# Optimization experiments

Measured on AMD Instinct MI355X. Metric: run time of the kernel, lower is better.

The kernel has to match this reference:

```python
import jax, jax.numpy as jnp
import numpy as np

HIDDEN = 256
N_PROT = 12288
N_MOL = 6144
N_BATCH = 32


def setup_inputs() -> dict:
    key = jax.random.key(0)
    ks = jax.random.split(key, 10)
    s = 1.0 / np.sqrt(HIDDEN)  # torch Linear default init scale
    inp = {
        "prot_embed": jax.random.normal(ks[0], (N_PROT, HIDDEN), jnp.float32),
        "mol_embed": jax.random.normal(ks[1], (N_MOL, HIDDEN), jnp.float32),
        "prot_batch": jnp.sort(jax.random.randint(ks[2], (N_PROT,), 0, N_BATCH)),
        "mol_batch": jnp.sort(jax.random.randint(ks[3], (N_MOL,), 0, N_BATCH)),
        "Wq": jax.random.uniform(ks[4], (HIDDEN, HIDDEN), jnp.float32, -s, s),
        "bq": jax.random.uniform(ks[5], (HIDDEN,), jnp.float32, -s, s),
        "Wk": jax.random.uniform(ks[6], (HIDDEN, HIDDEN), jnp.float32, -s, s),
        "bk": jax.random.uniform(ks[7], (HIDDEN,), jnp.float32, -s, s),
        "Wv": jax.random.uniform(ks[8], (HIDDEN, HIDDEN), jnp.float32, -s, s),
        "bv": jax.random.uniform(ks[9], (HIDDEN,), jnp.float32, -s, s),
    }
    return inp


def reference(prot_embed, mol_embed, prot_batch, mol_batch, Wq, bq, Wk, bk, Wv, bv):
    # Linear projections (torch nn.Linear: x @ W.T + b)
    Q = prot_embed @ Wq.T + bq            # [N, H]
    K = mol_embed @ Wk.T + bk             # [M, H]
    V = mol_embed @ Wv.T + bv             # [M, H]

    scale = 1.0 / jnp.sqrt(jnp.asarray(Q.shape[-1], Q.dtype))
    scores = (Q @ K.T) * scale            # [N, M]

    # block mask: same-batch pairs only
    mask = prot_batch[:, None] == mol_batch[None, :]   # [N, M] bool
    neg_inf = jnp.asarray(-jnp.inf, scores.dtype)
    scores = jnp.where(mask, scores, neg_inf)

    # stable masked softmax; rows with no valid key -> all zeros
    # (matches torch softmax(-inf row) -> nan -> nan_to_num(0.0))
    row_any = mask.any(axis=-1, keepdims=True)
    mx = jnp.max(scores, axis=-1, keepdims=True)
    mx = jnp.where(row_any, mx, 0.0)
    e = jnp.exp(scores - mx)              # exp(-inf)=0 on masked entries
    denom = jnp.sum(e, axis=-1, keepdims=True)
    attn = e / jnp.where(row_any, denom, 1.0)  # [N, M]

    out = attn @ V                        # [N, H]
    return out, attn
```

## Files before the change

kernel.cpp:

```cpp
#include <hip/hip_runtime.h>

#define NPROT 12288
#define NMOL  6144
#define HID   256
#define NB    32

#define PROT_O 0
#define MOL_O  3145728
#define WQ_O   4718592
#define WK_O   4784128
#define WV_O   4849664
#define BQ_O   4915200
#define BK_O   4915456
#define BV_O   4915712
#define Q_O    4915968
#define K_O    8061696
#define VT_O   9634560
#define END_O  11207424

#define FILL_BLOCKS 512
#define FILL_CHUNK  73728
#define FILL_HALF   37748736

typedef __attribute__((ext_vector_type(4))) float f32x4;
typedef __attribute__((ext_vector_type(8))) short bf16x8;
typedef unsigned short u16;
typedef unsigned int   u32;

__device__ __forceinline__ float b2f(u16 u){
  union { u32 i; float f; } v; v.i = ((u32)u) << 16; return v.f;
}
__device__ __forceinline__ u16 f2b(float f){
  union { float fl; u32 i; } v; v.fl = f;
  u32 i = v.i;
  return (u16)((i + 0x7FFFu + ((i >> 16) & 1u)) >> 16);
}

__device__ __forceinline__ void fill_zero(float* attnf, int idx){
  float* dst = attnf + (size_t)idx * FILL_CHUNK + threadIdx.x * 4;
  f32x4 z = {0.f, 0.f, 0.f, 0.f};
  #pragma unroll 4
  for (int i = 0; i < 72; i++)
    __builtin_nontemporal_store(z, (f32x4*)(dst + i * 1024));
}

__global__ __launch_bounds__(256) void convert_kernel(
    const float* __restrict__ prot, const float* __restrict__ mol,
    const float* __restrict__ Wq, const float* __restrict__ Wk,
    const float* __restrict__ Wv, const float* __restrict__ bq,
    const float* __restrict__ bk, const float* __restrict__ bv,
    const int* __restrict__ pb, const int* __restrict__ mb,
    int* __restrict__ rg, u16* __restrict__ cvt, float* __restrict__ dout)
{
  if (blockIdx.x >= 4801){
    fill_zero(dout + (size_t)NPROT * HID, blockIdx.x - 4801);
    return;
  }
  int g = blockIdx.x * 256 + threadIdx.x;
  const float* src = nullptr; u16* dst = nullptr; int off = 0;
  if      (g < 786432)  { src = prot; dst = cvt + PROT_O; off = g; }
  else if (g < 1179648) { src = mol;  dst = cvt + MOL_O;  off = g - 786432; }
  else if (g < 1196032) { src = Wq;   dst = cvt + WQ_O;   off = g - 1179648; }
  else if (g < 1212416) { src = Wk;   dst = cvt + WK_O;   off = g - 1196032; }
  else if (g < 1228800) { src = Wv;   dst = cvt + WV_O;   off = g - 1212416; }
  else if (g < 1228864) { src = bq;   dst = cvt + BQ_O;   off = g - 1228800; }
  else if (g < 1228928) { src = bk;   dst = cvt + BK_O;   off = g - 1228864; }
  else if (g < 1228992) { src = bv;   dst = cvt + BV_O;   off = g - 1228928; }
  if (src){
    f32x4 v = *(const f32x4*)(src + (size_t)off * 4);
    ushort4 o;
    o.x = f2b(v[0]); o.y = f2b(v[1]); o.z = f2b(v[2]); o.w = f2b(v[3]);
    *(ushort4*)(dst + (size_t)off * 4) = o;
  }

  if (blockIdx.x == 0 && threadIdx.x < 64){
    int t = threadIdx.x;
    const int* arr = (t < 32) ? pb : mb;
    int n          = (t < 32) ? NPROT : NMOL;
    int target     = (t & 31) + 1;
    int lo = 0, hi = n;
    while (lo < hi){
      int mid = (lo + hi) >> 1;
      if (arr[mid] < target) lo = mid + 1; else hi = mid;
    }
    int end = lo;
    int prev = __shfl(end, t - 1);
    int start = ((t & 31) == 0) ? 0 : prev;
    int b = t & 31;
    if (t < 32){ rg[b] = start; rg[32 + b] = end; }
    else       { rg[64 + b] = start; rg[96 + b] = end; }
  }
}

__global__ __launch_bounds__(256) void proj_kernel(
    const u16* __restrict__ cvt,
    u16* __restrict__ Q, u16* __restrict__ K, u16* __restrict__ Vt,
    float* __restrict__ dout)
{
  __shared__ u16 tlds[4][64][18];
  if (blockIdx.x >= 1536){
    fill_zero(dout + (size_t)NPROT * HID + FILL_HALF, blockIdx.x - 1536);
    return;
  }
  int rowblk = blockIdx.x >> 2, colblk = blockIdx.x & 3;
  int proj;
  if      (rowblk < 192){ proj = 0; }
  else if (rowblk < 288){ proj = 1; rowblk -= 192; }
  else                  { proj = 2; rowblk -= 288; }
  const u16 *X, *W, *B;
  if (proj == 0){ X = cvt + PROT_O; W = cvt + WQ_O; B = cvt + BQ_O; }
  else if (proj == 1){ X = cvt + MOL_O; W = cvt + WK_O; B = cvt + BK_O; }
  else { X = cvt + MOL_O; W = cvt + WV_O; B = cvt + BV_O; }

  int wave = threadIdx.x >> 6, lane = threadIdx.x & 63;
  int m = lane & 15, q = lane >> 4;
  int rowbase = rowblk * 64 + wave * 16;
  int colbase = colblk * 64;

  const u16* arow = X + (size_t)(rowbase + m) * HID;
  f32x4 acc[4] = {};
  for (int k0 = 0; k0 < HID; k0 += 32){
    bf16x8 a = *(const bf16x8*)(arow + k0 + q*8);
    #pragma unroll
    for (int ct = 0; ct < 4; ct++){
      bf16x8 b = *(const bf16x8*)(W + (size_t)(colbase + ct*16 + m) * HID + k0 + q*8);
      acc[ct] = __builtin_amdgcn_mfma_f32_16x16x32_bf16(a, b, acc[ct], 0, 0, 0);
    }
  }

  if (proj < 2){
    u16* O = (proj == 0) ? Q : K;
    #pragma unroll
    for (int ct = 0; ct < 4; ct++){
      int col = colbase + ct*16 + m;
      float bb = b2f(B[col]);
      #pragma unroll
      for (int r = 0; r < 4; r++){
        int row = rowbase + q*4 + r;
        O[(size_t)row * HID + col] = f2b(acc[ct][r] + bb);
      }
    }
  } else {
    #pragma unroll
    for (int ct = 0; ct < 4; ct++){
      int lc = ct*16 + m;
      float bb = b2f(B[colbase + lc]);
      #pragma unroll
      for (int r = 0; r < 4; r++)
        tlds[wave][lc][q*4 + r] = f2b(acc[ct][r] + bb);
    }
    __syncthreads();
    int col = colbase + lane;
    u32 packed[8];
    #pragma unroll
    for (int i = 0; i < 8; i++){
      u16 lo = tlds[wave][lane][2*i];
      u16 hi = tlds[wave][lane][2*i+1];
      packed[i] = (u32)lo | ((u32)hi << 16);
    }
    u16* dst = Vt + (size_t)col * NMOL + rowbase;
    uint4 v0 = {packed[0], packed[1], packed[2], packed[3]};
    uint4 v1 = {packed[4], packed[5], packed[6], packed[7]};
    *(uint4*)dst = v0;
    *(uint4*)(dst + 8) = v1;
  }
}

__global__ __launch_bounds__(256) void attn_kernel(
    const int* __restrict__ rg, const u16* __restrict__ Q, const u16* __restrict__ K,
    const u16* __restrict__ Vt, float* __restrict__ dout)
{
  __shared__ u16 P[16][392];
  __shared__ float mxw[4][16];
  __shared__ float smw[4][16];
  const float scale = 0.0625f;
  int b = blockIdx.y;
  int ps = rg[b], pe = rg[32+b], ms = rg[64+b], me = rg[96+b];
  int Np = pe - ps, Nm = me - ms;
  if (Np <= 0) return;

  int wave = threadIdx.x >> 6, lane = threadIdx.x & 63;
  int m = lane & 15, q = lane >> 4;
  float* outf  = dout;
  float* attnf = dout + (size_t)NPROT * HID;
  int ntiles = (Np + 15) >> 4;

  int bs = 0, ce = 0;
  if (Nm > 0){ bs = ms & ~31; ce = bs + ((me - bs + 31) & ~31); }

  for (int tile = blockIdx.x; tile < ntiles; tile += gridDim.x){
    int row0 = ps + tile * 16;
    int qr = min(row0 + m, NPROT - 1);
    const u16* qrow = Q + (size_t)qr * HID;
    bf16x8 qf[8];
    #pragma unroll
    for (int kk = 0; kk < 8; kk++)
      qf[kk] = *(const bf16x8*)(qrow + kk*32 + q*8);

    if (Nm > 0){
      int myj0 = bs + wave * 16;
      f32x4 sreg[6];
      float mx[4] = {-1e30f, -1e30f, -1e30f, -1e30f};
      #pragma unroll
      for (int c = 0; c < 6; c++){
        int j0 = myj0 + 64*c;
        if (j0 < ce){
          int col = j0 + m;
          bool valid = (col >= ms) && (col < me);
          const u16* krow = K + (size_t)col * HID;
          f32x4 s0 = {0.f,0.f,0.f,0.f}, s1 = {0.f,0.f,0.f,0.f};
          #pragma unroll
          for (int kk = 0; kk < 4; kk++){
            bf16x8 kb0 = *(const bf16x8*)(krow + kk*32 + q*8);
            bf16x8 kb1 = *(const bf16x8*)(krow + (kk+4)*32 + q*8);
            s0 = __builtin_amdgcn_mfma_f32_16x16x32_bf16(qf[kk],   kb0, s0, 0, 0, 0);
            s1 = __builtin_amdgcn_mfma_f32_16x16x32_bf16(qf[kk+4], kb1, s1, 0, 0, 0);
          }
          f32x4 sv;
          #pragma unroll
          for (int r = 0; r < 4; r++)
            sv[r] = valid ? (s0[r] + s1[r]) * scale : -1e30f;
          sreg[c] = sv;
          float cm[4];
          #pragma unroll
          for (int r = 0; r < 4; r++) cm[r] = sv[r];
          #pragma unroll
          for (int d = 1; d < 16; d <<= 1)
            #pragma unroll
            for (int r = 0; r < 4; r++)
              cm[r] = fmaxf(cm[r], __shfl_xor(cm[r], d, 16));
          #pragma unroll
          for (int r = 0; r < 4; r++) mx[r] = fmaxf(mx[r], cm[r]);
        }
      }
      if (m == 0){
        #pragma unroll
        for (int r = 0; r < 4; r++) mxw[wave][q*4 + r] = mx[r];
      }
      __syncthreads();
      float gmx[4];
      #pragma unroll
      for (int r = 0; r < 4; r++){
        int row = q*4 + r;
        float M = mxw[0][row];
        #pragma unroll
        for (int w = 1; w < 4; w++) M = fmaxf(M, mxw[w][row]);
        gmx[r] = M;
      }

      float sm[4] = {0.f, 0.f, 0.f, 0.f};
      #pragma unroll
      for (int c = 0; c < 6; c++){
        int j0 = myj0 + 64*c;
        if (j0 < ce){
          f32x4 e;
          #pragma unroll
          for (int r = 0; r < 4; r++) e[r] = __expf(sreg[c][r] - gmx[r]);
          sreg[c] = e;
          float t[4];
          #pragma unroll
          for (int r = 0; r < 4; r++) t[r] = e[r];
          #pragma unroll
          for (int d = 1; d < 16; d <<= 1)
            #pragma unroll
            for (int r = 0; r < 4; r++)
              t[r] += __shfl_xor(t[r], d, 16);
          #pragma unroll
          for (int r = 0; r < 4; r++) sm[r] += t[r];
        }
      }
      if (m == 0){
        #pragma unroll
        for (int r = 0; r < 4; r++) smw[wave][q*4 + r] = sm[r];
      }
      __syncthreads();
      float ginv[4];
      #pragma unroll
      for (int r = 0; r < 4; r++){
        int row = q*4 + r;
        float S = smw[0][row] + smw[1][row] + smw[2][row] + smw[3][row];
        ginv[r] = (S > 0.f) ? (1.f / S) : 0.f;
      }

      #pragma unroll
      for (int c = 0; c < 6; c++){
        int j0 = myj0 + 64*c;
        if (j0 < ce){
          int col = j0 + m;
          int jl = j0 - bs;
          bool valid = (col >= ms) && (col < me);
          #pragma unroll
          for (int r = 0; r < 4; r++){
            float p = sreg[c][r] * ginv[r];
            P[q*4 + r][jl + m] = f2b(p);
            int row = row0 + q*4 + r;
            if (valid && row < pe)
              __builtin_nontemporal_store(p, attnf + (size_t)row * NMOL + col);
          }
        }
      }
      __syncthreads();

      f32x4 oacc[4] = {};
      for (int j0 = bs; j0 < ce; j0 += 32){
        int jl = j0 - bs;
        bf16x8 a = *(const bf16x8*)(&P[m][jl + q*8]);
        #pragma unroll
        for (int c2 = 0; c2 < 4; c2++){
          int ct = wave*4 + c2;
          bf16x8 vb = *(const bf16x8*)(Vt + (size_t)(ct*16 + m) * NMOL + j0 + q*8);
          oacc[c2] = __builtin_amdgcn_mfma_f32_16x16x32_bf16(a, vb, oacc[c2], 0, 0, 0);
        }
      }
      #pragma unroll
      for (int c2 = 0; c2 < 4; c2++){
        int col = (wave*4 + c2)*16 + m;
        #pragma unroll
        for (int r = 0; r < 4; r++){
          int row = row0 + q*4 + r;
          if (row < pe) outf[(size_t)row * HID + col] = oacc[c2][r];
        }
      }
    } else {
      #pragma unroll
      for (int c2 = 0; c2 < 4; c2++){
        int col = (wave*4 + c2)*16 + m;
        #pragma unroll
        for (int r = 0; r < 4; r++){
          int row = row0 + q*4 + r;
          if (row < pe) outf[(size_t)row * HID + col] = 0.f;
        }
      }
    }
    __syncthreads();
  }
}

extern "C" void kernel_launch(void* const* d_in, const int* in_sizes, int n_in,
                              void* d_out, int out_size, void* d_ws, size_t ws_size,
                              hipStream_t stream)
{
  (void)in_sizes; (void)n_in; (void)out_size;
  const float* prot = (const float*)d_in[0];
  const float* mol  = (const float*)d_in[1];
  const int* pb     = (const int*)d_in[2];
  const int* mb     = (const int*)d_in[3];
  const float* Wq   = (const float*)d_in[4];
  const float* bq   = (const float*)d_in[5];
  const float* Wk   = (const float*)d_in[6];
  const float* bk   = (const float*)d_in[7];
  const float* Wv   = (const float*)d_in[8];
  const float* bv   = (const float*)d_in[9];

  const size_t need = 1024 + (size_t)END_O * 2;
  if (ws_size < need) return;

  char* ws = (char*)d_ws;
  int* rg  = (int*)ws;
  u16* cvt = (u16*)(ws + 1024);
  u16* Qp  = cvt + Q_O;
  u16* Kp  = cvt + K_O;
  u16* Vtp = cvt + VT_O;
  float* out = (float*)d_out;

  convert_kernel<<<dim3(4801 + FILL_BLOCKS), dim3(256), 0, stream>>>(
      prot, mol, Wq, Wk, Wv, bq, bk, bv, pb, mb, rg, cvt, out);
  proj_kernel<<<dim3(1536 + FILL_BLOCKS), dim3(256), 0, stream>>>(
      cvt, Qp, Kp, Vtp, out);
  attn_kernel<<<dim3(32, NB), dim3(256), 0, stream>>>(rg, Qp, Kp, Vtp, out);
}
```

Measured before the change: 407.4 us.

## Zero only off-block attention entries for last third of rows inside attention kernel

The full zero-fill of the attention matrix is split: the convert and proj kernels now zero the first 8192 rows entirely, in 8-row chunks. The remaining 4096 rows are zeroed by extra blocks in the attention kernel, which skip each row's same-batch column range because the attention pass writes it anyway. This cuts redundant zero stores and moves part of the fill so it overlaps with attention compute. In exchange it adds per-row batch lookups and some unaligned scalar stores at the range edges.

New measurement: 390.1 us. 1.04x faster.

```diff
diff --git a/kernel.cpp b/kernel.cpp
--- a/kernel.cpp
+++ b/kernel.cpp
@@ -18,9 +18,7 @@
 #define VT_O   9634560
 #define END_O  11207424
 
-#define FILL_BLOCKS 512
-#define FILL_CHUNK  73728
-#define FILL_HALF   37748736
+#define FROWS_BLK 49152
 
 typedef __attribute__((ext_vector_type(4))) float f32x4;
 typedef __attribute__((ext_vector_type(8))) short bf16x8;
@@ -36,11 +34,11 @@
   return (u16)((i + 0x7FFFu + ((i >> 16) & 1u)) >> 16);
 }
 
-__device__ __forceinline__ void fill_zero(float* attnf, int idx){
-  float* dst = attnf + (size_t)idx * FILL_CHUNK + threadIdx.x * 4;
+__device__ __forceinline__ void fill_rows8(float* attnf, int fid){
+  float* dst = attnf + (size_t)fid * FROWS_BLK + threadIdx.x * 4;
   f32x4 z = {0.f, 0.f, 0.f, 0.f};
   #pragma unroll 4
-  for (int i = 0; i < 72; i++)
+  for (int i = 0; i < 48; i++)
     __builtin_nontemporal_store(z, (f32x4*)(dst + i * 1024));
 }
 
@@ -53,7 +51,7 @@
     int* __restrict__ rg, u16* __restrict__ cvt, float* __restrict__ dout)
 {
   if (blockIdx.x >= 4801){
-    fill_zero(dout + (size_t)NPROT * HID, blockIdx.x - 4801);
+    fill_rows8(dout + (size_t)NPROT * HID, blockIdx.x - 4801);
     return;
   }
   int g = blockIdx.x * 256 + threadIdx.x;
@@ -99,7 +97,7 @@
 {
   __shared__ u16 tlds[4][64][18];
   if (blockIdx.x >= 1536){
-    fill_zero(dout + (size_t)NPROT * HID + FILL_HALF, blockIdx.x - 1536);
+    fill_rows8(dout + (size_t)NPROT * HID, blockIdx.x - 1536 + 512);
     return;
   }
   int rowblk = blockIdx.x >> 2, colblk = blockIdx.x & 3;
@@ -167,13 +165,40 @@
 }
 
 __global__ __launch_bounds__(256) void attn_kernel(
-    const int* __restrict__ rg, const u16* __restrict__ Q, const u16* __restrict__ K,
+    const int* __restrict__ rg, const int* __restrict__ pb,
+    const u16* __restrict__ Q, const u16* __restrict__ K,
     const u16* __restrict__ Vt, float* __restrict__ dout)
 {
   __shared__ u16 P[16][392];
   __shared__ float mxw[4][16];
   __shared__ float smw[4][16];
   const float scale = 0.0625f;
+  float* outf  = dout;
+  float* attnf = dout + (size_t)NPROT * HID;
+
+  if (blockIdx.x >= 32){
+    int fid = (blockIdx.x - 32) + 8 * blockIdx.y;
+    int r0 = 8192 + fid * 16;
+    f32x4 z = {0.f, 0.f, 0.f, 0.f};
+    for (int rr = 0; rr < 16; rr++){
+      int row = r0 + rr;
+      int bb = pb[row];
+      int ms = rg[64 + bb], me = rg[96 + bb];
+      float* rowp = attnf + (size_t)row * NMOL;
+      int mv = ms & ~3;
+      for (int c = threadIdx.x * 4; c < mv; c += 1024)
+        __builtin_nontemporal_store(z, (f32x4*)(rowp + c));
+      for (int c = mv + threadIdx.x; c < ms; c += 256)
+        rowp[c] = 0.f;
+      int mu = (me + 3) & ~3;
+      for (int c = me + threadIdx.x; c < mu && c < NMOL; c += 256)
+        rowp[c] = 0.f;
+      for (int c = mu + threadIdx.x * 4; c < NMOL; c += 1024)
+        __builtin_nontemporal_store(z, (f32x4*)(rowp + c));
+    }
+    return;
+  }
+
   int b = blockIdx.y;
   int ps = rg[b], pe = rg[32+b], ms = rg[64+b], me = rg[96+b];
   int Np = pe - ps, Nm = me - ms;
@@ -181,14 +206,12 @@
 
   int wave = threadIdx.x >> 6, lane = threadIdx.x & 63;
   int m = lane & 15, q = lane >> 4;
-  float* outf  = dout;
-  float* attnf = dout + (size_t)NPROT * HID;
   int ntiles = (Np + 15) >> 4;
 
   int bs = 0, ce = 0;
   if (Nm > 0){ bs = ms & ~31; ce = bs + ((me - bs + 31) & ~31); }
 
-  for (int tile = blockIdx.x; tile < ntiles; tile += gridDim.x){
+  for (int tile = blockIdx.x; tile < ntiles; tile += 32){
     int row0 = ps + tile * 16;
     int qr = min(row0 + m, NPROT - 1);
     const u16* qrow = Q + (size_t)qr * HID;
@@ -363,9 +386,9 @@
   u16* Vtp = cvt + VT_O;
   float* out = (float*)d_out;
 
-  convert_kernel<<<dim3(4801 + FILL_BLOCKS), dim3(256), 0, stream>>>(
+  convert_kernel<<<dim3(4801 + 512), dim3(256), 0, stream>>>(
       prot, mol, Wq, Wk, Wv, bq, bk, bv, pb, mb, rg, cvt, out);
-  proj_kernel<<<dim3(1536 + FILL_BLOCKS), dim3(256), 0, stream>>>(
+  proj_kernel<<<dim3(1536 + 512), dim3(256), 0, stream>>>(
       cvt, Qp, Kp, Vtp, out);
-  attn_kernel<<<dim3(32, NB), dim3(256), 0, stream>>>(rg, Qp, Kp, Vtp, out);
-}
+  attn_kernel<<<dim3(40, NB), dim3(256), 0, stream>>>(rg, pb, Qp, Kp, Vtp, out);
+}
```
